# Kernel tuning notes

Hardware: AMD Instinct MI355X
Metric: run time of the kernel (lower is better)

Reference implementation:

```python
import jax, jax.numpy as jnp
import numpy as np

D_MODEL = 1024
D_Q = 1024
D_V = 1024


def setup_inputs() -> dict:
    key = jax.random.key(0)
    k0, k1, k2, k3 = jax.random.split(key, 4)
    embedding_word = jax.random.normal(k0, (4, 2048, D_MODEL), dtype=jnp.float32)
    # nn.Linear weights are [out, in]; we store transposed [in, out] for x @ W
    s = 1.0 / np.sqrt(D_MODEL)
    w_q = jax.random.uniform(k1, (D_MODEL, D_Q), jnp.float32, -s, s)
    w_k = jax.random.uniform(k2, (D_MODEL, D_Q), jnp.float32, -s, s)
    w_v = jax.random.uniform(k3, (D_MODEL, D_V), jnp.float32, -s, s)
    return {"embedding_word": embedding_word, "w_q": w_q, "w_k": w_k, "w_v": w_v}


def reference(embedding_word, w_q, w_k, w_v):
    # q,k: [B,T,d_q]; v: [B,T,d_v]
    q = embedding_word @ w_q
    k = embedding_word @ w_k
    v = embedding_word @ w_v
    scores = jnp.einsum("btd,bsd->bts", q, k)  # [B,T,T]
    T = scores.shape[-1]
    causal = jnp.tril(jnp.ones((T, T), dtype=bool))  # True = keep
    masked = jnp.where(causal, scores, -jnp.inf)
    weights = jax.nn.softmax(masked / jnp.sqrt(jnp.float32(D_Q)), axis=-1)
    return jnp.einsum("bts,bsv->btv", weights, v)
```

## Files before the change

kernel.cpp:

```cpp
#include <hip/hip_runtime.h>
#include <cstdint>

typedef __bf16 bf16_t;
typedef __attribute__((ext_vector_type(8))) __bf16 bf16x8;
typedef __attribute__((ext_vector_type(4))) __bf16 bf16x4;
typedef __attribute__((ext_vector_type(4))) float f32x4;

#define AS1 __attribute__((address_space(1)))
#define AS3 __attribute__((address_space(3)))

template <typename OutT, int TAG, int SWAPXY>
__global__ __launch_bounds__(256)
void gemm_nt(const bf16_t* __restrict__ A, const bf16_t* __restrict__ B,
             OutT* __restrict__ C, int K, int lda, int ldb, int ldc)
{
  const int bm = SWAPXY ? blockIdx.x : blockIdx.y;
  const int bn = SWAPXY ? blockIdx.y : blockIdx.x;
  const int m0 = bm * 128, n0 = bn * 128;

  __shared__ bf16_t As[2][128 * 64];
  __shared__ bf16_t Bs[2][128 * 64];

  const int tid = threadIdx.x;
  const int wave = tid >> 6, lane = tid & 63;
  const int lm = lane & 15, qd = lane >> 4;
  const int wm = (wave >> 1) * 64, wn = (wave & 1) * 64;

  const int rowl = lane >> 3;
  const int q = (lane & 7) ^ rowl;
  const bf16_t* Abase = A + (long)(m0 + wave * 8 + rowl) * lda + q * 8;
  const bf16_t* Bbase = B + (long)(n0 + wave * 8 + rowl) * ldb + q * 8;
  const int woff = wave * 512;

  auto stage = [&](int k0, int b) {
#pragma unroll
    for (int i = 0; i < 4; i++) {
      __builtin_amdgcn_global_load_lds((const AS1 void*)(Abase + (long)i * 32 * lda + k0),
                                       (AS3 void*)(As[b] + woff + i * 2048), 16, 0, 0);
      __builtin_amdgcn_global_load_lds((const AS1 void*)(Bbase + (long)i * 32 * ldb + k0),
                                       (AS3 void*)(Bs[b] + woff + i * 2048), 16, 0, 0);
    }
  };

  f32x4 acc[4][4] = {};

  stage(0, 0);
  int buf = 0;
  for (int k0 = 0; k0 < K; k0 += 64) {
    __syncthreads();
    if (k0 + 64 < K) stage(k0 + 64, buf ^ 1);
#pragma unroll
    for (int s = 0; s < 2; s++) {
      bf16x8 aF[4], bF[4];
#pragma unroll
      for (int i = 0; i < 4; i++) {
        const int r = wm + i * 16 + lm;
        aF[i] = *(const bf16x8*)&As[buf][r * 64 + (((s * 4 + qd) ^ (lm & 7)) << 3)];
      }
#pragma unroll
      for (int j = 0; j < 4; j++) {
        const int r = wn + j * 16 + lm;
        bF[j] = *(const bf16x8*)&Bs[buf][r * 64 + (((s * 4 + qd) ^ (lm & 7)) << 3)];
      }
#pragma unroll
      for (int i = 0; i < 4; i++)
#pragma unroll
        for (int j = 0; j < 4; j++)
          acc[i][j] = __builtin_amdgcn_mfma_f32_16x16x32_bf16(aF[i], bF[j], acc[i][j], 0, 0, 0);
    }
    buf ^= 1;
  }

#pragma unroll
  for (int i = 0; i < 4; i++) {
    const int row = m0 + wm + i * 16 + qd * 4;
#pragma unroll
    for (int j = 0; j < 4; j++) {
      const int col = n0 + wn + j * 16 + lm;
#pragma unroll
      for (int r = 0; r < 4; r++)
        C[(long)(row + r) * ldc + col] = (OutT)acc[i][j][r];
    }
  }
}

template <typename OutT, int TAG>
__global__ __launch_bounds__(256)
void gemm_ntc(const bf16_t* __restrict__ A, const bf16_t* __restrict__ B,
              OutT* __restrict__ C, int K, int lda, int ldb, int ldc,
              long sA, long sB, long sC, int causal, int kLimit)
{
  int bm = blockIdx.y;
  const int bn = blockIdx.x;
  if (kLimit) bm = gridDim.y - 1 - bm;
  if (causal && bn > bm) return;
  A += (long)blockIdx.z * sA;
  B += (long)blockIdx.z * sB;
  C += (long)blockIdx.z * sC;
  const int m0 = bm * 128, n0 = bn * 128;
  int Keff = K;
  if (kLimit) { const int kl = (bm + 1) * 128; if (kl < Keff) Keff = kl; }

  __shared__ bf16_t As[2][128 * 64];
  __shared__ bf16_t Bs[2][128 * 64];

  const int tid = threadIdx.x;
  const int wave = tid >> 6, lane = tid & 63;
  const int lm = lane & 15, qd = lane >> 4;
  const int wm = (wave >> 1) * 64, wn = (wave & 1) * 64;

  const int rowl = lane >> 3;
  const int q = (lane & 7) ^ rowl;
  const bf16_t* Abase = A + (long)(m0 + wave * 8 + rowl) * lda + q * 8;
  const bf16_t* Bbase = B + (long)(n0 + wave * 8 + rowl) * ldb + q * 8;
  const int woff = wave * 512;

  auto stage = [&](int k0, int b) {
#pragma unroll
    for (int i = 0; i < 4; i++) {
      __builtin_amdgcn_global_load_lds((const AS1 void*)(Abase + (long)i * 32 * lda + k0),
                                       (AS3 void*)(As[b] + woff + i * 2048), 16, 0, 0);
      __builtin_amdgcn_global_load_lds((const AS1 void*)(Bbase + (long)i * 32 * ldb + k0),
                                       (AS3 void*)(Bs[b] + woff + i * 2048), 16, 0, 0);
    }
  };

  f32x4 acc[4][4] = {};

  stage(0, 0);
  int buf = 0;
  for (int k0 = 0; k0 < Keff; k0 += 64) {
    __syncthreads();
    if (k0 + 64 < Keff) stage(k0 + 64, buf ^ 1);
#pragma unroll
    for (int s = 0; s < 2; s++) {
      bf16x8 aF[4], bF[4];
#pragma unroll
      for (int i = 0; i < 4; i++) {
        const int r = wm + i * 16 + lm;
        aF[i] = *(const bf16x8*)&As[buf][r * 64 + (((s * 4 + qd) ^ (lm & 7)) << 3)];
      }
#pragma unroll
      for (int j = 0; j < 4; j++) {
        const int r = wn + j * 16 + lm;
        bF[j] = *(const bf16x8*)&Bs[buf][r * 64 + (((s * 4 + qd) ^ (lm & 7)) << 3)];
      }
#pragma unroll
      for (int i = 0; i < 4; i++)
#pragma unroll
        for (int j = 0; j < 4; j++)
          acc[i][j] = __builtin_amdgcn_mfma_f32_16x16x32_bf16(aF[i], bF[j], acc[i][j], 0, 0, 0);
    }
    buf ^= 1;
  }

#pragma unroll
  for (int i = 0; i < 4; i++) {
    const int row = m0 + wm + i * 16 + qd * 4;
#pragma unroll
    for (int j = 0; j < 4; j++) {
      const int col = n0 + wn + j * 16 + lm;
#pragma unroll
      for (int r = 0; r < 4; r++)
        C[(long)(row + r) * ldc + col] = (OutT)acc[i][j][r];
    }
  }
}

__global__ __launch_bounds__(256)
void prep(const float* __restrict__ X, bf16_t* __restrict__ Xb,
          const float* __restrict__ wq, const float* __restrict__ wk,
          const float* __restrict__ wv, bf16_t* __restrict__ WT)
{
  const int b = blockIdx.x;
  if (b < 8192) {
    const int i = b * 256 + threadIdx.x;
    const float4 f = ((const float4*)X)[i];
    bf16x4 o = {(bf16_t)f.x, (bf16_t)f.y, (bf16_t)f.z, (bf16_t)f.w};
    ((bf16x4*)Xb)[i] = o;
    return;
  }
  const int wid = b - 8192;
  const int z = wid >> 10;
  const int t = wid & 1023;
  const int tix = t & 31, tiy = t >> 5;
  const float* W = (z == 0) ? wq : (z == 1) ? wk : wv;
  bf16_t* O = WT + (long)z * 1024 * 1024;

  __shared__ float tile[32][33];
  const int x = threadIdx.x & 31, y0 = threadIdx.x >> 5;
#pragma unroll
  for (int r = 0; r < 4; r++) {
    const int y = y0 + r * 8;
    tile[y][x] = W[(long)(tiy * 32 + y) * 1024 + (tix * 32 + x)];
  }
  __syncthreads();
#pragma unroll
  for (int r = 0; r < 4; r++) {
    const int y = y0 + r * 8;
    O[(long)(tix * 32 + y) * 1024 + (tiy * 32 + x)] = (bf16_t)tile[x][y];
  }
}

__global__ __launch_bounds__(256)
void softmax_causal(bf16_t* __restrict__ S)
{
  const int row = blockIdx.x;
  const int t = row & 2047;
  const int kend = ((t >> 7) + 1) << 7;
  bf16_t* Sr = S + (long)row * 2048;
  const int base = threadIdx.x * 8;

  uint4 u = {0, 0, 0, 0};
  if (base <= t) u = *(const uint4*)(Sr + base);
  const unsigned short* up = (const unsigned short*)&u;
  float v[8];
  float m = -3.0e38f;
#pragma unroll
  for (int j = 0; j < 8; j++) {
    const float x = __uint_as_float(((unsigned)up[j]) << 16);
    v[j] = (base + j <= t) ? x : -3.0e38f;
    m = fmaxf(m, v[j]);
  }
#pragma unroll
  for (int off = 32; off > 0; off >>= 1) m = fmaxf(m, __shfl_xor(m, off));
  __shared__ float redm[4], redl[4];
  const int wave = threadIdx.x >> 6, lane = threadIdx.x & 63;
  if (lane == 0) redm[wave] = m;
  __syncthreads();
  m = fmaxf(fmaxf(redm[0], redm[1]), fmaxf(redm[2], redm[3]));

  float p[8], l = 0.f;
#pragma unroll
  for (int j = 0; j < 8; j++) {
    p[j] = (base + j <= t) ? __expf((v[j] - m) * 0.03125f) : 0.f;
    l += p[j];
  }
#pragma unroll
  for (int off = 32; off > 0; off >>= 1) l += __shfl_xor(l, off);
  if (lane == 0) redl[wave] = l;
  __syncthreads();
  l = (redl[0] + redl[1]) + (redl[2] + redl[3]);
  const float rl = 1.0f / l;

  if (base < kend) {
    uint4 w;
    unsigned* wp = (unsigned*)&w;
#pragma unroll
    for (int h = 0; h < 4; h++) {
      bf16_t a = (bf16_t)(p[2 * h] * rl);
      bf16_t b = (bf16_t)(p[2 * h + 1] * rl);
      wp[h] = (unsigned)__builtin_bit_cast(unsigned short, a) |
              ((unsigned)__builtin_bit_cast(unsigned short, b) << 16);
    }
    *(uint4*)(Sr + base) = w;
  }
}

extern "C" void kernel_launch(void* const* d_in, const int* in_sizes, int n_in,
                              void* d_out, int out_size, void* d_ws, size_t ws_size,
                              hipStream_t stream)
{
  const float* X  = (const float*)d_in[0];
  const float* Wq = (const float*)d_in[1];
  const float* Wk = (const float*)d_in[2];
  const float* Wv = (const float*)d_in[3];
  float* out = (float*)d_out;

  char* p = (char*)d_ws;
  bf16_t* QK = (bf16_t*)p;  p += (size_t)8192 * 2048 * 2;
  bf16_t* VT = (bf16_t*)p;  p += (size_t)1024 * 8192 * 2;
  bf16_t* WT = (bf16_t*)p;  p += (size_t)3072 * 1024 * 2;
  bf16_t* Xb = (bf16_t*)p;
  bf16_t* S  = (bf16_t*)p;

  prep<<<8192 + 3072, 256, 0, stream>>>(X, Xb, Wq, Wk, Wv, WT);
  gemm_nt<bf16_t, 2, 1><<<dim3(64, 16), 256, 0, stream>>>(
      Xb, WT, QK, 1024, 1024, 1024, 2048);
  gemm_nt<bf16_t, 3, 0><<<dim3(64, 8), 256, 0, stream>>>(
      WT + (long)2048 * 1024, Xb, VT, 1024, 1024, 1024, 8192);
  gemm_ntc<bf16_t, 4><<<dim3(16, 16, 4), 256, 0, stream>>>(
      QK, QK + 1024, S, 1024, 2048, 2048, 2048,
      (long)2048 * 2048, (long)2048 * 2048, (long)2048 * 2048, 1, 0);
  softmax_causal<<<8192, 256, 0, stream>>>(S);
  gemm_ntc<float, 6><<<dim3(8, 16, 4), 256, 0, stream>>>(
      S, VT, out, 2048, 2048, 8192, 1024,
      (long)2048 * 2048, 2048, (long)2048 * 1024, 0, 1);
}
```

Baseline: 249.2 us.

## Launch triangular grid for causal scores, grid-stride cast, balance PV tile order

The causal QK^T GEMM now launches only the 136 lower-triangular tiles per batch and maps each linear block index to (row, col) with a sqrt-based inversion, so half-empty blocks are no longer launched and then exited. The fp32-to-bf16 input cast uses a grid-stride loop over 2048 blocks instead of one block per 256 float4s, which cuts block scheduling overhead. The PV GEMM reverses the row-tile order only for half of the batches, so heavy and light K-limited tiles are interleaved across the grid. The triangular index math adds a few scalar ops per block.

```diff
diff --git a/kernel.cpp b/kernel.cpp
--- a/kernel.cpp
+++ b/kernel.cpp
@@ -1,5 +1,6 @@
 #include <hip/hip_runtime.h>
 #include <cstdint>
+#include <cmath>
 
 typedef __bf16 bf16_t;
 typedef __attribute__((ext_vector_type(8))) __bf16 bf16x8;
@@ -84,22 +85,30 @@
   }
 }
 
-template <typename OutT, int TAG>
+template <typename OutT, int TAG, int TRI>
 __global__ __launch_bounds__(256)
 void gemm_ntc(const bf16_t* __restrict__ A, const bf16_t* __restrict__ B,
               OutT* __restrict__ C, int K, int lda, int ldb, int ldc,
-              long sA, long sB, long sC, int causal, int kLimit)
-{
-  int bm = blockIdx.y;
-  const int bn = blockIdx.x;
-  if (kLimit) bm = gridDim.y - 1 - bm;
-  if (causal && bn > bm) return;
+              long sA, long sB, long sC, int kLimit)
+{
+  int bm, bn;
+  if (TRI) {
+    const int j = blockIdx.x;
+    bm = (int)((sqrtf(8.f * j + 1.f) - 1.f) * 0.5f);
+    while ((bm + 1) * (bm + 2) / 2 <= j) bm++;
+    while (bm * (bm + 1) / 2 > j) bm--;
+    bn = j - bm * (bm + 1) / 2;
+  } else {
+    bn = blockIdx.x;
+    bm = blockIdx.y;
+    if (kLimit) bm = (blockIdx.z & 2) ? bm : (gridDim.y - 1 - bm);
+  }
   A += (long)blockIdx.z * sA;
   B += (long)blockIdx.z * sB;
   C += (long)blockIdx.z * sC;
   const int m0 = bm * 128, n0 = bn * 128;
   int Keff = K;
-  if (kLimit) { const int kl = (bm + 1) * 128; if (kl < Keff) Keff = kl; }
+  if (!TRI && kLimit) { const int kl = (bm + 1) * 128; if (kl < Keff) Keff = kl; }
 
   __shared__ bf16_t As[2][128 * 64];
   __shared__ bf16_t Bs[2][128 * 64];
@@ -173,14 +182,17 @@
           const float* __restrict__ wv, bf16_t* __restrict__ WT)
 {
   const int b = blockIdx.x;
-  if (b < 8192) {
-    const int i = b * 256 + threadIdx.x;
-    const float4 f = ((const float4*)X)[i];
-    bf16x4 o = {(bf16_t)f.x, (bf16_t)f.y, (bf16_t)f.z, (bf16_t)f.w};
-    ((bf16x4*)Xb)[i] = o;
+  if (b < 2048) {
+    const int N4 = 8192 * 1024 / 4;
+    const int stride = 2048 * 256;
+    for (int i = b * 256 + threadIdx.x; i < N4; i += stride) {
+      const float4 f = ((const float4*)X)[i];
+      bf16x4 o = {(bf16_t)f.x, (bf16_t)f.y, (bf16_t)f.z, (bf16_t)f.w};
+      ((bf16x4*)Xb)[i] = o;
+    }
     return;
   }
-  const int wid = b - 8192;
+  const int wid = b - 2048;
   const int z = wid >> 10;
   const int t = wid & 1023;
   const int tix = t & 31, tiy = t >> 5;
@@ -274,16 +286,16 @@
   bf16_t* Xb = (bf16_t*)p;
   bf16_t* S  = (bf16_t*)p;
 
-  prep<<<8192 + 3072, 256, 0, stream>>>(X, Xb, Wq, Wk, Wv, WT);
+  prep<<<2048 + 3072, 256, 0, stream>>>(X, Xb, Wq, Wk, Wv, WT);
   gemm_nt<bf16_t, 2, 1><<<dim3(64, 16), 256, 0, stream>>>(
       Xb, WT, QK, 1024, 1024, 1024, 2048);
   gemm_nt<bf16_t, 3, 0><<<dim3(64, 8), 256, 0, stream>>>(
       WT + (long)2048 * 1024, Xb, VT, 1024, 1024, 1024, 8192);
-  gemm_ntc<bf16_t, 4><<<dim3(16, 16, 4), 256, 0, stream>>>(
+  gemm_ntc<bf16_t, 4, 1><<<dim3(136, 1, 4), 256, 0, stream>>>(
       QK, QK + 1024, S, 1024, 2048, 2048, 2048,
-      (long)2048 * 2048, (long)2048 * 2048, (long)2048 * 2048, 1, 0);
+      (long)2048 * 2048, (long)2048 * 2048, (long)2048 * 2048, 0);
   softmax_causal<<<8192, 256, 0, stream>>>(S);
-  gemm_ntc<float, 6><<<dim3(8, 16, 4), 256, 0, stream>>>(
+  gemm_ntc<float, 6, 0><<<dim3(8, 16, 4), 256, 0, stream>>>(
       S, VT, out, 2048, 2048, 8192, 1024,
-      (long)2048 * 2048, 2048, (long)2048 * 1024, 0, 1);
-}
+      (long)2048 * 2048, 2048, (long)2048 * 1024, 1);
+}
```

Measured after the change: 247.5 us. Within noise of the previous version (-0.7%).
